# Kernel tuning notes

Hardware: AMD Instinct MI355X
Metric: run time of the kernel (lower is better)

Reference implementation:

```python
import jax, jax.numpy as jnp
import numpy as np

F = 65536          # num_face
W_DIM = 512
PAD = 4096         # zero pad rows appended before gather
LRELU_SLOPE = 0.2
LRELU_GAIN = np.sqrt(2.0).astype(np.float32)  # def_gain of lrelu


def _fc(w, W, b):
    # StyleGAN FullyConnectedLayer: x @ W.T / sqrt(in_features) + bias
    gain = np.float32(1.0 / np.sqrt(W.shape[1]))
    return w @ W.T * gain + b


def _faceconv_gather(x, neigh, is_pad, k):
    # x: [B*F, C]; neigh/is_pad: [B*F, 9]; take first k neighbor slots.
    padded = jnp.concatenate([x, jnp.zeros((PAD, x.shape[1]), x.dtype)], axis=0)
    g = padded[neigh[:, :k]]                      # [B*F, k, C] irregular gather
    return jnp.where(is_pad[:, :k, None], jnp.zeros((), x.dtype), g)


def _modulated_face_conv(g, weight, styles, demodulate):
    # g: [B*F, k, I]; weight: [O, I, 1, k]; styles: [B, I]
    B = styles.shape[0]
    w = weight[None, :, :, 0, :] * styles[:, None, :, None]      # [B, O, I, k]
    if demodulate:
        d = jax.lax.rsqrt(jnp.sum(w * w, axis=(2, 3)) + 1e-8)    # [B, O]
        w = w * d[:, :, None, None]
    gb = g.reshape(B, -1, g.shape[1], g.shape[2])                # [B, F, k, I]
    out = jnp.einsum('bfki,boik->bfo', gb, w)                    # [B, F, O]
    return out.reshape(-1, w.shape[1])


def setup_inputs() -> dict:
    key = jax.random.key(0)
    ks = jax.random.split(key, 12)
    B = 2
    C = 128
    N = B * F
    face_neighborhood = jax.random.randint(ks[0], (N, 9), 0, N + PAD, dtype=jnp.int64)
    face_is_pad = jax.random.randint(ks[1], (N, 9), 0, 10) == 0
    return {
        'face_neighborhood': face_neighborhood,
        'face_is_pad': face_is_pad,
        'ws': jax.random.normal(ks[2], (B, 2, W_DIM), jnp.float32),
        'const': jax.random.normal(ks[3], (F, C), jnp.float32),
        'affine1_W': jax.random.normal(ks[4], (C, W_DIM), jnp.float32),
        'affine1_b': jnp.ones((C,), jnp.float32),
        'weight1': jax.random.normal(ks[5], (C, C, 1, 9), jnp.float32),
        'noise_const': jax.random.normal(ks[6], (F,), jnp.float32),
        'noise_strength': jnp.zeros((1,), jnp.float32),
        'bias1': jnp.zeros((C,), jnp.float32),
        'affine2_W': jax.random.normal(ks[7], (C, W_DIM), jnp.float32),
        'affine2_b': jnp.ones((C,), jnp.float32),
        'weight2': jax.random.normal(ks[8], (3, C, 1, 1), jnp.float32),
        'bias2': jnp.zeros((3,), jnp.float32),
    }


def reference(face_neighborhood, face_is_pad, ws, const, affine1_W, affine1_b,
              weight1, noise_const, noise_strength, bias1, affine2_W, affine2_b,
              weight2, bias2):
    # noise_mode == 'const'
    B = ws.shape[0]
    w0, w1 = ws[:, 0], ws[:, 1]
    x = jnp.tile(const[None], (B, 1, 1)).reshape(B * F, -1)        # [B*F, C]

    # --- SynthesisLayer conv1 ---
    styles = _fc(w0, affine1_W, affine1_b)                         # [B, C]
    noise = jnp.tile(noise_const[None], (B, 1)).reshape(-1, 1) * noise_strength
    g = _faceconv_gather(x, face_neighborhood, face_is_pad, 9)     # [B*F, 9, C]
    x = _modulated_face_conv(g, weight1, styles, demodulate=True)  # [B*F, C]
    x = x + noise
    x = jax.nn.leaky_relu(x + bias1[None, :], LRELU_SLOPE)
    x = jnp.clip(x * LRELU_GAIN, -256.0, 256.0)                    # clamp_gain

    # --- ToRGBLayer ---
    wg = np.float32(1.0 / np.sqrt(weight2.shape[1] * 1))
    styles2 = _fc(w1, affine2_W, affine2_b) * wg
    g2 = _faceconv_gather(x, face_neighborhood, face_is_pad, 1)    # [B*F, 1, C]
    img = _modulated_face_conv(g2, weight2, styles2, demodulate=False)
    img = jnp.clip(img + bias2[None, :], -256.0, 256.0)
    return x, img
```

## Files before the change

### kernel.cpp

```cpp
#include <hip/hip_runtime.h>

typedef unsigned short u16;
typedef __bf16 bf16x8 __attribute__((ext_vector_type(8)));
typedef float f32x4 __attribute__((ext_vector_type(4)));
typedef unsigned short u16x8 __attribute__((ext_vector_type(8)));

#define F_FACES 65536
#define N_FACES 131072
#define C_CH 128
#define WS_W2F 256
#define WS_S1 3328
#define WS_S2 4352
#define WS_W1 5376
#define WS_CONST 595200
#define XELEMS 16777216

__device__ inline u16 f2bf(float f) {
    unsigned u = __builtin_bit_cast(unsigned, f);
    unsigned r = (u + 0x7fffu + ((u >> 16) & 1u)) >> 16;
    return (u16)r;
}

__device__ inline void gl_lds16(const void* g, void* l) {
    __builtin_amdgcn_global_load_lds(
        (const __attribute__((address_space(1))) void*)g,
        (__attribute__((address_space(3))) void*)l, 16, 0, 0);
}

__global__ __launch_bounds__(256) void k0a_styles(
    const float* __restrict__ wsv, const float* __restrict__ a1W, const float* __restrict__ a1b,
    const float* __restrict__ a2W, const float* __restrict__ a2b, unsigned char* __restrict__ wsb)
{
    int wv = threadIdx.x >> 6, lane = threadIdx.x & 63;
    int c = blockIdx.x * 4 + wv;
    int which = c >> 8, rem = c & 255, b = rem >> 7, o = rem & 127;
    const float* W = (which ? a2W : a1W) + o * 512 + lane * 8;
    const float* x = wsv + (b * 2 + which) * 512 + lane * 8;
    float4 wa = *(const float4*)(W);
    float4 wb = *(const float4*)(W + 4);
    float4 xa = *(const float4*)(x);
    float4 xb = *(const float4*)(x + 4);
    float s = wa.x * xa.x + wa.y * xa.y + wa.z * xa.z + wa.w * xa.w
            + wb.x * xb.x + wb.y * xb.y + wb.z * xb.z + wb.w * xb.w;
#pragma unroll
    for (int d = 1; d < 64; d <<= 1) s += __shfl_xor(s, d);
    if (lane == 0) {
        const float g512 = 0.04419417382415922f;
        const float g128 = 0.08838834764831845f;
        float* wsf = (float*)wsb;
        if (which == 0) {
            wsf[WS_S1 / 4 + b * 128 + o] = s * g512 + a1b[o];
        } else {
            wsf[WS_S2 / 4 + b * 128 + o] = (s * g512 + a2b[o]) * g128;
        }
    }
}

__global__ __launch_bounds__(256) void k0w_fold2(
    const float* __restrict__ w2, unsigned char* __restrict__ wsb)
{
    int t = threadIdx.x;
    float* wsf = (float*)wsb;
    if (t < 64) wsf[t] = 0.f;
#pragma unroll
    for (int r = 0; r < 3; ++r) {
        int id = t + r * 256;
        int b2 = id / 384;
        int rem = id - b2 * 384;
        int o2 = rem >> 7;
        int i = rem & 127;
        wsf[WS_W2F / 4 + id] = w2[o2 * 128 + i] * wsf[WS_S2 / 4 + b2 * 128 + i];
    }
}

__global__ __launch_bounds__(64) void k0b_fold(
    const float* __restrict__ w1g, const unsigned char* __restrict__ wsb, u16* __restrict__ w1out)
{
    int bo = blockIdx.x;
    int b = bo >> 7, o = bo & 127;
    int l = threadIdx.x;
    const float* s1 = (const float*)(wsb + WS_S1) + b * 128;
    float sum = 0.f;
    for (int e = l; e < 1152; e += 64) {
        int i = e / 9;
        float w = w1g[o * 1152 + e] * s1[i];
        sum += w * w;
    }
#pragma unroll
    for (int d = 1; d < 64; d <<= 1) sum += __shfl_xor(sum, d);
    float dm = rsqrtf(sum + 1e-8f);
    int i0 = l * 2;
    float sa = s1[i0] * dm, sb = s1[i0 + 1] * dm;
    int chunk = i0 >> 3, j = i0 & 7;
#pragma unroll
    for (int k = 0; k < 9; ++k) {
        float v0 = w1g[(o * 128 + i0) * 9 + k] * sa;
        float v1 = w1g[(o * 128 + i0 + 1) * 9 + k] * sb;
        unsigned pack = (unsigned)f2bf(v0) | ((unsigned)f2bf(v1) << 16);
        *(unsigned*)&w1out[(size_t)((((b * 9 + k) * 16 + chunk) * 128 + o) * 8 + j)] = pack;
    }
}

__global__ __launch_bounds__(256) void k_cvt(
    const float* __restrict__ src, u16* __restrict__ dst)
{
    int t = blockIdx.x * 256 + threadIdx.x;
    int base = t * 8;
    float4 a = *(const float4*)(src + base);
    float4 c = *(const float4*)(src + base + 4);
    u16x8 p;
    p[0] = f2bf(a.x); p[1] = f2bf(a.y); p[2] = f2bf(a.z); p[3] = f2bf(a.w);
    p[4] = f2bf(c.x); p[5] = f2bf(c.y); p[6] = f2bf(c.z); p[7] = f2bf(c.w);
    *(u16x8*)(dst + base) = p;
}

__global__ __launch_bounds__(256, 4) void k1_conv(
    const int* __restrict__ neigh, const int* __restrict__ ispad,
    const float* __restrict__ noise_c, const float* __restrict__ nstr,
    const float* __restrict__ bias1, const unsigned char* __restrict__ wsb,
    float* __restrict__ out)
{
    __shared__ u16 As[128 * 128];

    int tid = threadIdx.x;
    int wv = tid >> 6, lane = tid & 63;
    int quad = lane >> 4, l15 = lane & 15;
    int f0 = blockIdx.x * 128;
    int b = f0 >> 16;
    const u16* cst = (const u16*)(wsb + WS_CONST);
    const u16* w1ws = (const u16*)(wsb + WS_W1) + (size_t)b * 147456;
    const char* zp = (const char*)wsb;

    f32x4 acc[4][4] = {};
    int wm = wv & 1, wn = wv >> 1;

    for (int k = 0; k < 9; ++k) {
        __syncthreads();
#pragma unroll
        for (int r = 0; r < 8; ++r) {
            int cid = ((wv * 8 + r) << 6) + lane;
            int row = cid >> 4;
            int slot = cid & 15;
            int nb = (f0 + row) * 9 + k;
            int idx = neigh[nb];
            bool valid = (ispad[nb] == 0) && ((unsigned)idx < 131072u);
            const char* src = valid ? ((const char*)(cst + ((size_t)(idx & 65535) << 7))) : zp;
            gl_lds16(src + ((slot ^ (row & 15)) << 4), (char*)As + ((wv * 8 + r) << 10));
        }
        __syncthreads();
#pragma unroll
        for (int s = 0; s < 4; ++s) {
            bf16x8 af[4], bfr[4];
#pragma unroll
            for (int mt = 0; mt < 4; ++mt) {
                int face = wm * 64 + mt * 16 + l15;
                int chunk = (s * 4 + quad) ^ (face & 15);
                af[mt] = *reinterpret_cast<const bf16x8*>(&As[face * 128 + chunk * 8]);
            }
            const u16* bp = w1ws + (((k * 16 + s * 4 + quad) * 128) + wn * 64 + l15) * 8;
#pragma unroll
            for (int nt = 0; nt < 4; ++nt)
                bfr[nt] = *reinterpret_cast<const bf16x8*>(bp + nt * 128);
#pragma unroll
            for (int mt = 0; mt < 4; ++mt)
#pragma unroll
                for (int nt = 0; nt < 4; ++nt)
                    acc[mt][nt] = __builtin_amdgcn_mfma_f32_16x16x32_bf16(
                        af[mt], bfr[nt], acc[mt][nt], 0, 0, 0);
        }
    }

    float ns = nstr[0];
    float b1v[4];
#pragma unroll
    for (int nt = 0; nt < 4; ++nt) b1v[nt] = bias1[wn * 64 + nt * 16 + l15];
#pragma unroll
    for (int mt = 0; mt < 4; ++mt) {
#pragma unroll
        for (int r = 0; r < 4; ++r) {
            int face = f0 + wm * 64 + mt * 16 + quad * 4 + r;
            float nz = noise_c[face & 65535] * ns;
#pragma unroll
            for (int nt = 0; nt < 4; ++nt) {
                float v = acc[mt][nt][r] + nz + b1v[nt];
                v = (v > 0.f) ? v : 0.2f * v;
                v *= 1.41421356f;
                v = fminf(fmaxf(v, -256.f), 256.f);
                out[(size_t)face * 128 + wn * 64 + nt * 16 + l15] = v;
            }
        }
    }
}

__global__ __launch_bounds__(256) void k2_img(
    const int* __restrict__ neigh, const int* __restrict__ ispad,
    const float* __restrict__ w2f, const float* __restrict__ bias2,
    const float* __restrict__ xbuf, float* __restrict__ imgout)
{
    __shared__ float ws2[768];
    int tid = threadIdx.x;
    ws2[tid] = w2f[tid];
    ws2[tid + 256] = w2f[tid + 256];
    ws2[tid + 512] = w2f[tid + 512];
    __syncthreads();
    int wv = tid >> 6, lane = tid & 63;
    int g = lane >> 4, sub = lane & 15;
    int face = blockIdx.x * 16 + wv * 4 + g;
    int b = face >> 16;
    int idx = neigh[face * 9];
    bool valid = (ispad[face * 9] == 0) && ((unsigned)idx < 131072u);
    float a0 = 0.f, a1 = 0.f, a2 = 0.f;
    if (valid) {
        float4 d0 = *(const float4*)(xbuf + (size_t)idx * 128 + sub * 8);
        float4 d1 = *(const float4*)(xbuf + (size_t)idx * 128 + sub * 8 + 4);
        float f[8] = {d0.x, d0.y, d0.z, d0.w, d1.x, d1.y, d1.z, d1.w};
        const float* w0 = &ws2[(b * 3 + 0) * 128 + sub * 8];
        const float* w1 = &ws2[(b * 3 + 1) * 128 + sub * 8];
        const float* w2p = &ws2[(b * 3 + 2) * 128 + sub * 8];
#pragma unroll
        for (int j = 0; j < 8; ++j) {
            a0 += f[j] * w0[j];
            a1 += f[j] * w1[j];
            a2 += f[j] * w2p[j];
        }
    }
#pragma unroll
    for (int d = 1; d < 16; d <<= 1) {
        a0 += __shfl_xor(a0, d);
        a1 += __shfl_xor(a1, d);
        a2 += __shfl_xor(a2, d);
    }
    if (sub < 3) {
        float v = (sub == 0) ? a0 : (sub == 1) ? a1 : a2;
        v += bias2[sub];
        v = fminf(fmaxf(v, -256.f), 256.f);
        imgout[face * 3 + sub] = v;
    }
}

extern "C" void kernel_launch(void* const* d_in, const int* in_sizes, int n_in,
                              void* d_out, int out_size, void* d_ws, size_t ws_size,
                              hipStream_t stream) {
    const int* neigh = (const int*)d_in[0];
    const int* ispad = (const int*)d_in[1];
    const float* wsv = (const float*)d_in[2];
    const float* cst = (const float*)d_in[3];
    const float* a1W = (const float*)d_in[4];
    const float* a1b = (const float*)d_in[5];
    const float* w1g = (const float*)d_in[6];
    const float* noise_c = (const float*)d_in[7];
    const float* nstr = (const float*)d_in[8];
    const float* bias1 = (const float*)d_in[9];
    const float* a2W = (const float*)d_in[10];
    const float* a2b = (const float*)d_in[11];
    const float* w2 = (const float*)d_in[12];
    const float* bias2 = (const float*)d_in[13];
    float* out = (float*)d_out;
    unsigned char* wsb = (unsigned char*)d_ws;

    k0a_styles<<<128, 256, 0, stream>>>(wsv, a1W, a1b, a2W, a2b, wsb);
    k0w_fold2<<<1, 256, 0, stream>>>(w2, wsb);
    k0b_fold<<<256, 64, 0, stream>>>(w1g, wsb, (u16*)(wsb + WS_W1));
    k_cvt<<<4096, 256, 0, stream>>>(cst, (u16*)(wsb + WS_CONST));
    k1_conv<<<1024, 256, 0, stream>>>(neigh, ispad, noise_c, nstr, bias1, wsb, out);
    k2_img<<<8192, 256, 0, stream>>>(neigh, ispad, (const float*)(wsb + WS_W2F), bias2,
                                     out, out + XELEMS);
}
```

Baseline: 235.4 us.

## Double-buffer gather tiles in conv kernel, widen block, fuse prep kernels

```diff
diff --git a/kernel.cpp b/kernel.cpp
--- a/kernel.cpp
+++ b/kernel.cpp
@@ -56,15 +56,57 @@
     }
 }
 
-__global__ __launch_bounds__(256) void k0w_fold2(
+__global__ __launch_bounds__(256) void k0f_fused(
+    const float* __restrict__ cst, const float* __restrict__ w1g,
     const float* __restrict__ w2, unsigned char* __restrict__ wsb)
 {
-    int t = threadIdx.x;
+    __shared__ float red[4];
+    int bid = blockIdx.x;
+    int tid = threadIdx.x;
+
+    if (bid < 4096) {
+        u16* dst = (u16*)(wsb + WS_CONST);
+        int base = (bid * 256 + tid) * 8;
+        float4 a = *(const float4*)(cst + base);
+        float4 c = *(const float4*)(cst + base + 4);
+        u16x8 p;
+        p[0] = f2bf(a.x); p[1] = f2bf(a.y); p[2] = f2bf(a.z); p[3] = f2bf(a.w);
+        p[4] = f2bf(c.x); p[5] = f2bf(c.y); p[6] = f2bf(c.z); p[7] = f2bf(c.w);
+        *(u16x8*)(dst + base) = p;
+        return;
+    }
+    if (bid < 4352) {
+        int bo = bid - 4096;
+        int b = bo >> 7, o = bo & 127;
+        const float* s1 = (const float*)(wsb + WS_S1) + b * 128;
+        float sum = 0.f;
+        for (int e = tid; e < 1152; e += 256) {
+            int i = e / 9;
+            float w = w1g[o * 1152 + e] * s1[i];
+            sum += w * w;
+        }
+        int wv = tid >> 6, lane = tid & 63;
+#pragma unroll
+        for (int d = 1; d < 64; d <<= 1) sum += __shfl_xor(sum, d);
+        if (lane == 0) red[wv] = sum;
+        __syncthreads();
+        float dm = rsqrtf(red[0] + red[1] + red[2] + red[3] + 1e-8f);
+        u16* w1out = (u16*)(wsb + WS_W1);
+        for (int wd = tid; wd < 576; wd += 256) {
+            int k = wd >> 6;
+            int ii = (wd & 63) * 2;
+            float v0 = w1g[(o * 128 + ii) * 9 + k] * s1[ii] * dm;
+            float v1 = w1g[(o * 128 + ii + 1) * 9 + k] * s1[ii + 1] * dm;
+            unsigned pack = (unsigned)f2bf(v0) | ((unsigned)f2bf(v1) << 16);
+            *(unsigned*)&w1out[(size_t)((((b * 9 + k) * 16 + (ii >> 3)) * 128 + o) * 8 + (ii & 7))] = pack;
+        }
+        return;
+    }
     float* wsf = (float*)wsb;
-    if (t < 64) wsf[t] = 0.f;
+    if (tid < 64) wsf[tid] = 0.f;
 #pragma unroll
     for (int r = 0; r < 3; ++r) {
-        int id = t + r * 256;
+        int id = tid + r * 256;
         int b2 = id / 384;
         int rem = id - b2 * 384;
         int o2 = rem >> 7;
@@ -73,107 +115,106 @@
     }
 }
 
-__global__ __launch_bounds__(64) void k0b_fold(
-    const float* __restrict__ w1g, const unsigned char* __restrict__ wsb, u16* __restrict__ w1out)
-{
-    int bo = blockIdx.x;
-    int b = bo >> 7, o = bo & 127;
-    int l = threadIdx.x;
-    const float* s1 = (const float*)(wsb + WS_S1) + b * 128;
-    float sum = 0.f;
-    for (int e = l; e < 1152; e += 64) {
-        int i = e / 9;
-        float w = w1g[o * 1152 + e] * s1[i];
-        sum += w * w;
-    }
-#pragma unroll
-    for (int d = 1; d < 64; d <<= 1) sum += __shfl_xor(sum, d);
-    float dm = rsqrtf(sum + 1e-8f);
-    int i0 = l * 2;
-    float sa = s1[i0] * dm, sb = s1[i0 + 1] * dm;
-    int chunk = i0 >> 3, j = i0 & 7;
-#pragma unroll
-    for (int k = 0; k < 9; ++k) {
-        float v0 = w1g[(o * 128 + i0) * 9 + k] * sa;
-        float v1 = w1g[(o * 128 + i0 + 1) * 9 + k] * sb;
-        unsigned pack = (unsigned)f2bf(v0) | ((unsigned)f2bf(v1) << 16);
-        *(unsigned*)&w1out[(size_t)((((b * 9 + k) * 16 + chunk) * 128 + o) * 8 + j)] = pack;
-    }
-}
-
-__global__ __launch_bounds__(256) void k_cvt(
-    const float* __restrict__ src, u16* __restrict__ dst)
-{
-    int t = blockIdx.x * 256 + threadIdx.x;
-    int base = t * 8;
-    float4 a = *(const float4*)(src + base);
-    float4 c = *(const float4*)(src + base + 4);
-    u16x8 p;
-    p[0] = f2bf(a.x); p[1] = f2bf(a.y); p[2] = f2bf(a.z); p[3] = f2bf(a.w);
-    p[4] = f2bf(c.x); p[5] = f2bf(c.y); p[6] = f2bf(c.z); p[7] = f2bf(c.w);
-    *(u16x8*)(dst + base) = p;
-}
-
-__global__ __launch_bounds__(256, 4) void k1_conv(
+__global__ __launch_bounds__(512, 4) void k1_conv(
     const int* __restrict__ neigh, const int* __restrict__ ispad,
     const float* __restrict__ noise_c, const float* __restrict__ nstr,
     const float* __restrict__ bias1, const unsigned char* __restrict__ wsb,
     float* __restrict__ out)
 {
-    __shared__ u16 As[128 * 128];
-
-    int tid = threadIdx.x;
-    int wv = tid >> 6, lane = tid & 63;
-    int quad = lane >> 4, l15 = lane & 15;
-    int f0 = blockIdx.x * 128;
-    int b = f0 >> 16;
+    __shared__ __align__(16) u16 As[2][128 * 128];
+
+    const int tid = threadIdx.x;
+    const int wv = tid >> 6, lane = tid & 63;
+    const int quad = lane >> 4, l15 = lane & 15;
+    const int f0 = blockIdx.x * 128;
+    const int b = f0 >> 16;
     const u16* cst = (const u16*)(wsb + WS_CONST);
     const u16* w1ws = (const u16*)(wsb + WS_W1) + (size_t)b * 147456;
     const char* zp = (const char*)wsb;
-
-    f32x4 acc[4][4] = {};
-    int wm = wv & 1, wn = wv >> 1;
-
+    const int wm = wv & 1, wn = wv >> 1;
+
+    f32x4 acc[4][2] = {};
+    int ia[4], ip[4];
+
+#pragma unroll
+    for (int r = 0; r < 4; ++r) {
+        int nb = (f0 + (wv * 4 + r) * 4 + quad) * 9 + 0;
+        ia[r] = neigh[nb]; ip[r] = ispad[nb];
+    }
+#pragma unroll
+    for (int r = 0; r < 4; ++r) {
+        int row = (wv * 4 + r) * 4 + quad;
+        bool valid = (ip[r] == 0) && ((unsigned)ia[r] < 131072u);
+        const char* src = valid ? (const char*)(cst + ((size_t)(ia[r] & 65535) << 7)) : zp;
+        gl_lds16(src + ((l15 ^ (row & 15)) << 4), (char*)(&As[0][0]) + ((wv * 4 + r) << 10));
+    }
+#pragma unroll
+    for (int r = 0; r < 4; ++r) {
+        int nb = (f0 + (wv * 4 + r) * 4 + quad) * 9 + 1;
+        ia[r] = neigh[nb]; ip[r] = ispad[nb];
+    }
+
+#pragma unroll
     for (int k = 0; k < 9; ++k) {
-        __syncthreads();
-#pragma unroll
-        for (int r = 0; r < 8; ++r) {
-            int cid = ((wv * 8 + r) << 6) + lane;
-            int row = cid >> 4;
-            int slot = cid & 15;
-            int nb = (f0 + row) * 9 + k;
-            int idx = neigh[nb];
-            bool valid = (ispad[nb] == 0) && ((unsigned)idx < 131072u);
-            const char* src = valid ? ((const char*)(cst + ((size_t)(idx & 65535) << 7))) : zp;
-            gl_lds16(src + ((slot ^ (row & 15)) << 4), (char*)As + ((wv * 8 + r) << 10));
-        }
-        __syncthreads();
+        bf16x8 bfr[4][2];
+#pragma unroll
+        for (int s = 0; s < 4; ++s)
+#pragma unroll
+            for (int nt = 0; nt < 2; ++nt)
+                bfr[s][nt] = *reinterpret_cast<const bf16x8*>(
+                    w1ws + (((k * 16 + s * 4 + quad) * 128) + wn * 32 + nt * 16 + l15) * 8);
+        asm volatile("" ::: "memory");
+        __builtin_amdgcn_sched_barrier(0);
+
+        if (k < 8) {
+#pragma unroll
+            for (int r = 0; r < 4; ++r) {
+                int row = (wv * 4 + r) * 4 + quad;
+                bool valid = (ip[r] == 0) && ((unsigned)ia[r] < 131072u);
+                const char* src = valid ? (const char*)(cst + ((size_t)(ia[r] & 65535) << 7)) : zp;
+                gl_lds16(src + ((l15 ^ (row & 15)) << 4),
+                         (char*)(&As[(k + 1) & 1][0]) + ((wv * 4 + r) << 10));
+            }
+        }
+        if (k < 7) {
+#pragma unroll
+            for (int r = 0; r < 4; ++r) {
+                int nb = (f0 + (wv * 4 + r) * 4 + quad) * 9 + (k + 2);
+                ia[r] = neigh[nb]; ip[r] = ispad[nb];
+            }
+        }
+        if (k < 7)       asm volatile("s_waitcnt vmcnt(20)" ::: "memory");
+        else if (k == 7) asm volatile("s_waitcnt vmcnt(12)" ::: "memory");
+        else             asm volatile("s_waitcnt vmcnt(8)" ::: "memory");
+        __builtin_amdgcn_s_barrier();
+        __builtin_amdgcn_sched_barrier(0);
+
+        const u16* Ab = &As[k & 1][0];
 #pragma unroll
         for (int s = 0; s < 4; ++s) {
-            bf16x8 af[4], bfr[4];
+            bf16x8 af[4];
 #pragma unroll
             for (int mt = 0; mt < 4; ++mt) {
                 int face = wm * 64 + mt * 16 + l15;
-                int chunk = (s * 4 + quad) ^ (face & 15);
-                af[mt] = *reinterpret_cast<const bf16x8*>(&As[face * 128 + chunk * 8]);
+                int chunk = (s * 4 + quad) ^ l15;
+                af[mt] = *reinterpret_cast<const bf16x8*>(&Ab[face * 128 + chunk * 8]);
             }
-            const u16* bp = w1ws + (((k * 16 + s * 4 + quad) * 128) + wn * 64 + l15) * 8;
-#pragma unroll
-            for (int nt = 0; nt < 4; ++nt)
-                bfr[nt] = *reinterpret_cast<const bf16x8*>(bp + nt * 128);
 #pragma unroll
             for (int mt = 0; mt < 4; ++mt)
 #pragma unroll
-                for (int nt = 0; nt < 4; ++nt)
+                for (int nt = 0; nt < 2; ++nt)
                     acc[mt][nt] = __builtin_amdgcn_mfma_f32_16x16x32_bf16(
-                        af[mt], bfr[nt], acc[mt][nt], 0, 0, 0);
-        }
+                        af[mt], bfr[s][nt], acc[mt][nt], 0, 0, 0);
+        }
+        asm volatile("s_waitcnt lgkmcnt(0)" ::: "memory");
+        __builtin_amdgcn_s_barrier();
+        __builtin_amdgcn_sched_barrier(0);
     }
 
     float ns = nstr[0];
-    float b1v[4];
-#pragma unroll
-    for (int nt = 0; nt < 4; ++nt) b1v[nt] = bias1[wn * 64 + nt * 16 + l15];
+    float b1v[2];
+    b1v[0] = bias1[wn * 32 + l15];
+    b1v[1] = bias1[wn * 32 + 16 + l15];
 #pragma unroll
     for (int mt = 0; mt < 4; ++mt) {
 #pragma unroll
@@ -181,12 +222,12 @@
             int face = f0 + wm * 64 + mt * 16 + quad * 4 + r;
             float nz = noise_c[face & 65535] * ns;
 #pragma unroll
-            for (int nt = 0; nt < 4; ++nt) {
+            for (int nt = 0; nt < 2; ++nt) {
                 float v = acc[mt][nt][r] + nz + b1v[nt];
                 v = (v > 0.f) ? v : 0.2f * v;
                 v *= 1.41421356f;
                 v = fminf(fmaxf(v, -256.f), 256.f);
-                out[(size_t)face * 128 + wn * 64 + nt * 16 + l15] = v;
+                out[(size_t)face * 128 + wn * 32 + nt * 16 + l15] = v;
             }
         }
     }
@@ -259,10 +300,8 @@
     unsigned char* wsb = (unsigned char*)d_ws;
 
     k0a_styles<<<128, 256, 0, stream>>>(wsv, a1W, a1b, a2W, a2b, wsb);
-    k0w_fold2<<<1, 256, 0, stream>>>(w2, wsb);
-    k0b_fold<<<256, 64, 0, stream>>>(w1g, wsb, (u16*)(wsb + WS_W1));
-    k_cvt<<<4096, 256, 0, stream>>>(cst, (u16*)(wsb + WS_CONST));
-    k1_conv<<<1024, 256, 0, stream>>>(neigh, ispad, noise_c, nstr, bias1, wsb, out);
+    k0f_fused<<<4353, 256, 0, stream>>>(cst, w1g, w2, wsb);
+    k1_conv<<<1024, 512, 0, stream>>>(neigh, ispad, noise_c, nstr, bias1, wsb, out);
     k2_img<<<8192, 256, 0, stream>>>(neigh, ispad, (const float*)(wsb + WS_W2F), bias2,
                                      out, out + XELEMS);
 }
```

Result: faster. 192.5 us (-18.2%).
